# Performance work log

Measured on AMD Instinct MI355X. Metric: run time of the kernel, lower is better.

Reference implementation:

```python
import jax, jax.numpy as jnp
import numpy as np

B, S, D, H = 2, 2048, 1024, 16
DEPTH = D // H

def setup_inputs() -> dict:
    key = jax.random.key(0)
    k1, k2, k3 = jax.random.split(key, 3)
    x = jax.random.normal(k1, (B, S, D), dtype=jnp.float32)
    # causal mask (1 = attend, 0 = blocked), broadcastable over batch/heads
    mask = jnp.tril(jnp.ones((S, S), dtype=jnp.int32))[None, None]
    W_qkv = jax.random.normal(k2, (D, 3 * D), dtype=jnp.float32) * (D ** -0.5)
    b_qkv = jnp.zeros((3 * D,), dtype=jnp.float32)
    W_out = jax.random.normal(k3, (D, D), dtype=jnp.float32) * (D ** -0.5)
    b_out = jnp.zeros((D,), dtype=jnp.float32)
    return {"x": x, "mask": mask, "W_qkv": W_qkv, "b_qkv": b_qkv,
            "W_out": W_out, "b_out": b_out}

def reference(x, mask, W_qkv, b_qkv, W_out, b_out):
    b, s, _ = x.shape
    qkv = x @ W_qkv + b_qkv                        # [b, s, 3D]
    qkv = qkv.reshape(b, s, H, 3 * DEPTH)          # matches torch reshape
    qkv = jnp.transpose(qkv, (0, 2, 1, 3))         # [b, h, s, 3*depth]
    q, k, v = jnp.split(qkv, 3, axis=-1)           # each [b, h, s, depth]
    scores = jnp.einsum('bhqd,bhkd->bhqk', q, k) / jnp.sqrt(jnp.float32(DEPTH))
    scores = jnp.where(mask == 0, -jnp.inf, scores)
    attn = jax.nn.softmax(scores, axis=-1)         # dropout: eval mode (identity)
    out = jnp.einsum('bhqk,bhkd->bhqd', attn, v)   # [b, h, s, depth]
    out = jnp.transpose(out, (0, 2, 1, 3)).reshape(b, s, D)
    return out @ W_out + b_out
```

## Files before the change

kernel.cpp:

```cpp
#include <hip/hip_runtime.h>

#define BB 2
#define SS 2048
#define DDIM 1024
#define HH 16
#define DEPTH 64
#define QKVN (3*DDIM)

typedef unsigned short u16;
typedef unsigned int u32;
typedef __attribute__((ext_vector_type(8))) short bf16x8;
typedef __attribute__((ext_vector_type(4))) float f32x4;

__device__ __forceinline__ u16 f2bf(float f){
  union{float f; u32 u;} z; z.f=f;
  u32 r = z.u + 0x7fffu + ((z.u>>16)&1u);
  return (u16)(r>>16);
}
#define NEG_BIG (-1e30f)

__global__ void convT_k(const float* __restrict__ in, u16* __restrict__ out, int R, int C){
  __shared__ float tile[32][33];
  int c0 = blockIdx.x<<5, r0 = blockIdx.y<<5;
  int tx = threadIdx.x, ty = threadIdx.y;
  for (int i=ty;i<32;i+=8) tile[i][tx] = in[(size_t)(r0+i)*C + c0+tx];
  __syncthreads();
  for (int i=ty;i<32;i+=8) out[(size_t)(c0+i)*R + r0+tx] = f2bf(tile[tx][i]);
}

__global__ void convX_k(const float* __restrict__ in, u16* __restrict__ out){
  size_t i = ((size_t)blockIdx.x*256 + threadIdx.x) * 8;
  float4 a = *(const float4*)(in + i);
  float4 b = *(const float4*)(in + i + 4);
  ushort4 lo = { f2bf(a.x), f2bf(a.y), f2bf(a.z), f2bf(a.w) };
  ushort4 hi = { f2bf(b.x), f2bf(b.y), f2bf(b.z), f2bf(b.w) };
  *(ushort4*)(out + i)     = lo;
  *(ushort4*)(out + i + 4) = hi;
}

__global__ __launch_bounds__(256,2) void gemm_qkv_k(
    const u16* __restrict__ A, const u16* __restrict__ Bt,
    const float* __restrict__ bias,
    u16* __restrict__ Qb, u16* __restrict__ Kb, u16* __restrict__ Vt)
{
  const int K = DDIM;
  __shared__ __align__(16) u16 As[128*32];
  __shared__ __align__(16) u16 Bs[128*32];
  const int tid = threadIdx.x;
  const int m0 = blockIdx.x<<7, n0 = blockIdx.y<<7;
  const int w = tid>>6, lane = tid&63, q = lane>>4, ln = lane&15;
  const int wr = (w>>1)<<6, wc = (w&1)<<6;

  f32x4 acc[4][4];
  #pragma unroll
  for (int i=0;i<4;i++)
    #pragma unroll
    for (int j=0;j<4;j++) acc[i][j] = (f32x4){0.f,0.f,0.f,0.f};

  for (int k0=0;k0<K;k0+=32){
    {
      int c = tid, row = c>>2, off = (c&3)<<3;
      *(uint4*)&As[(row<<5)+off] = *(const uint4*)&A [(size_t)(m0+row)*K + k0 + off];
      *(uint4*)&Bs[(row<<5)+off] = *(const uint4*)&Bt[(size_t)(n0+row)*K + k0 + off];
      c = tid + 256; row = c>>2; off = (c&3)<<3;
      *(uint4*)&As[(row<<5)+off] = *(const uint4*)&A [(size_t)(m0+row)*K + k0 + off];
      *(uint4*)&Bs[(row<<5)+off] = *(const uint4*)&Bt[(size_t)(n0+row)*K + k0 + off];
    }
    __syncthreads();
    bf16x8 af[4], bfr[4];
    #pragma unroll
    for (int i=0;i<4;i++) af[i]  = *(const bf16x8*)&As[((wr + (i<<4) + ln)<<5) + (q<<3)];
    #pragma unroll
    for (int j=0;j<4;j++) bfr[j] = *(const bf16x8*)&Bs[((wc + (j<<4) + ln)<<5) + (q<<3)];
    #pragma unroll
    for (int i=0;i<4;i++)
      #pragma unroll
      for (int j=0;j<4;j++)
        acc[i][j] = __builtin_amdgcn_mfma_f32_16x16x32_bf16(af[i], bfr[j], acc[i][j], 0, 0, 0);
    __syncthreads();
  }

  #pragma unroll
  for (int i=0;i<4;i++){
    const int mmb = m0 + wr + (i<<4) + (q<<2);
    const int bsel = mmb >> 11;
    const int sb   = mmb & 2047;
    #pragma unroll
    for (int j=0;j<4;j++){
      const int n = n0 + wc + (j<<4) + ln;
      const int h = n / 192;
      const int rr = n - h*192;
      const int bh = (bsel<<4) + h;
      const float bv = bias[n];
      if (rr < 64){
        u16* dst = Qb + (size_t)bh*SS*DEPTH + rr;
        #pragma unroll
        for (int r=0;r<4;r++) dst[(size_t)(sb+r)*DEPTH] = f2bf((acc[i][j][r] + bv)*0.125f);
      } else if (rr < 128){
        u16* dst = Kb + (size_t)bh*SS*DEPTH + (rr-64);
        #pragma unroll
        for (int r=0;r<4;r++) dst[(size_t)(sb+r)*DEPTH] = f2bf(acc[i][j][r] + bv);
      } else {
        ushort4 pv = { f2bf(acc[i][j][0] + bv), f2bf(acc[i][j][1] + bv),
                       f2bf(acc[i][j][2] + bv), f2bf(acc[i][j][3] + bv) };
        *(ushort4*)(Vt + ((size_t)bh*DEPTH + (rr-128))*SS + sb) = pv;
      }
    }
  }
}

__global__ __launch_bounds__(256,4) void attn_k(
    u16* __restrict__ Qb, const u16* __restrict__ Kb, const u16* __restrict__ Vt)
{
  __shared__ __align__(16) u16 Ks[64*72];
  __shared__ __align__(16) u16 VsT[64*72];
  __shared__ __align__(16) u16 ps[4][16*72];

  const int tid = threadIdx.x, w = tid>>6, lane = tid&63, q = lane>>4, ln = lane&15;
  const int bh = blockIdx.x;
  const int y  = blockIdx.y, sgrp = y>>3, rr_ = y&7;
  const int qt = (sgrp==0) ? 31-rr_ : (sgrp==1) ? 16+rr_ : (sgrp==2) ? 15-rr_ : rr_;
  const int r0 = qt<<6;
  const size_t kbase = (size_t)bh*SS*DEPTH;
  const size_t vbase = (size_t)bh*DEPTH*SS;

  bf16x8 qf[2];
  #pragma unroll
  for (int ks=0;ks<2;ks++)
    qf[ks] = *(const bf16x8*)(Qb + kbase + (size_t)(r0 + (w<<4) + ln)*DEPTH + (ks<<5) + (q<<3));

  f32x4 o[4];
  #pragma unroll
  for (int nt=0;nt<4;nt++) o[nt] = (f32x4){0.f,0.f,0.f,0.f};
  float m_r[4], l_r[4];
  #pragma unroll
  for (int r=0;r<4;r++){ m_r[r] = NEG_BIG; l_r[r] = 0.f; }

  const int T = qt + 1;
  for (int t=0;t<T;t++){
    __syncthreads();
    #pragma unroll
    for (int p=0;p<2;p++){
      int e = (p*256 + tid)*8;
      int j = e>>6, d = e&63;
      *(uint4*)&Ks[j*72 + d]   = *(const uint4*)(Kb + kbase + (size_t)((t<<6)+j)*DEPTH + d);
      *(uint4*)&VsT[j*72 + d]  = *(const uint4*)(Vt + vbase + (size_t)j*SS + (t<<6) + d);
    }
    __syncthreads();

    f32x4 sc[4];
    #pragma unroll
    for (int jt=0;jt<4;jt++) sc[jt] = (f32x4){0.f,0.f,0.f,0.f};
    #pragma unroll
    for (int ks=0;ks<2;ks++){
      #pragma unroll
      for (int jt=0;jt<4;jt++){
        bf16x8 kf = *(const bf16x8*)&Ks[((jt<<4)+ln)*72 + (ks<<5) + (q<<3)];
        sc[jt] = __builtin_amdgcn_mfma_f32_16x16x32_bf16(qf[ks], kf, sc[jt], 0, 0, 0);
      }
    }

    if (t == T-1){
      const int rowb = r0 + (w<<4) + (q<<2);
      #pragma unroll
      for (int jt=0;jt<4;jt++){
        const int col = (t<<6) + (jt<<4) + ln;
        #pragma unroll
        for (int r=0;r<4;r++)
          if (col > rowb + r) sc[jt][r] = NEG_BIG;
      }
    }

    float alpha_r[4];
    #pragma unroll
    for (int r=0;r<4;r++){
      float mt = fmaxf(fmaxf(sc[0][r], sc[1][r]), fmaxf(sc[2][r], sc[3][r]));
      #pragma unroll
      for (int off=1; off<16; off<<=1) mt = fmaxf(mt, __shfl_xor(mt, off));
      const float mnew = fmaxf(m_r[r], mt);
      alpha_r[r] = __expf(m_r[r] - mnew);
      float p0 = __expf(sc[0][r]-mnew), p1 = __expf(sc[1][r]-mnew);
      float p2 = __expf(sc[2][r]-mnew), p3 = __expf(sc[3][r]-mnew);
      const int mrow = (q<<2) + r;
      ps[w][mrow*72 +      ln] = f2bf(p0);
      ps[w][mrow*72 + 16 + ln] = f2bf(p1);
      ps[w][mrow*72 + 32 + ln] = f2bf(p2);
      ps[w][mrow*72 + 48 + ln] = f2bf(p3);
      float psum = (p0+p1)+(p2+p3);
      #pragma unroll
      for (int off=1; off<16; off<<=1) psum += __shfl_xor(psum, off);
      l_r[r] = l_r[r]*alpha_r[r] + psum;
      m_r[r] = mnew;
    }
    #pragma unroll
    for (int nt=0;nt<4;nt++)
      #pragma unroll
      for (int r=0;r<4;r++) o[nt][r] *= alpha_r[r];

    __syncthreads();

    #pragma unroll
    for (int ks=0;ks<2;ks++){
      bf16x8 pa = *(const bf16x8*)&ps[w][ln*72 + (ks<<5) + (q<<3)];
      #pragma unroll
      for (int nt=0;nt<4;nt++){
        bf16x8 vf = *(const bf16x8*)&VsT[((nt<<4)+ln)*72 + (ks<<5) + (q<<3)];
        o[nt] = __builtin_amdgcn_mfma_f32_16x16x32_bf16(pa, vf, o[nt], 0, 0, 0);
      }
    }
  }

  #pragma unroll
  for (int r=0;r<4;r++){
    const float rl = 1.f / fmaxf(l_r[r], 1e-30f);
    const int s = r0 + (w<<4) + (q<<2) + r;
    #pragma unroll
    for (int nt=0;nt<4;nt++)
      Qb[kbase + (size_t)s*DEPTH + (nt<<4) + ln] = f2bf(o[nt][r] * rl);
  }
}

__global__ __launch_bounds__(256,2) void gemm_out_k(
    const u16* __restrict__ Aq, const u16* __restrict__ Bt,
    const float* __restrict__ bias, float* __restrict__ out)
{
  const int K = DDIM;
  __shared__ __align__(16) u16 As[128*32];
  __shared__ __align__(16) u16 Bs[128*32];
  const int tid = threadIdx.x;
  const int m0 = blockIdx.x<<7, n0 = blockIdx.y<<7;
  const int bsel = m0>>11, ms = m0&2047;
  const int w = tid>>6, lane = tid&63, q = lane>>4, ln = lane&15;
  const int wr = (w>>1)<<6, wc = (w&1)<<6;

  f32x4 acc[4][4];
  #pragma unroll
  for (int i=0;i<4;i++)
    #pragma unroll
    for (int j=0;j<4;j++) acc[i][j] = (f32x4){0.f,0.f,0.f,0.f};

  for (int k0=0;k0<K;k0+=32){
    const size_t abase = (size_t)((bsel<<4) + (k0>>6))*SS*DEPTH + (k0&63);
    {
      int c = tid, row = c>>2, off = (c&3)<<3;
      *(uint4*)&As[(row<<5)+off] = *(const uint4*)&Aq[abase + (size_t)(ms+row)*DEPTH + off];
      *(uint4*)&Bs[(row<<5)+off] = *(const uint4*)&Bt[(size_t)(n0+row)*K + k0 + off];
      c = tid + 256; row = c>>2; off = (c&3)<<3;
      *(uint4*)&As[(row<<5)+off] = *(const uint4*)&Aq[abase + (size_t)(ms+row)*DEPTH + off];
      *(uint4*)&Bs[(row<<5)+off] = *(const uint4*)&Bt[(size_t)(n0+row)*K + k0 + off];
    }
    __syncthreads();
    bf16x8 af[4], bfr[4];
    #pragma unroll
    for (int i=0;i<4;i++) af[i]  = *(const bf16x8*)&As[((wr + (i<<4) + ln)<<5) + (q<<3)];
    #pragma unroll
    for (int j=0;j<4;j++) bfr[j] = *(const bf16x8*)&Bs[((wc + (j<<4) + ln)<<5) + (q<<3)];
    #pragma unroll
    for (int i=0;i<4;i++)
      #pragma unroll
      for (int j=0;j<4;j++)
        acc[i][j] = __builtin_amdgcn_mfma_f32_16x16x32_bf16(af[i], bfr[j], acc[i][j], 0, 0, 0);
    __syncthreads();
  }

  #pragma unroll
  for (int i=0;i<4;i++){
    #pragma unroll
    for (int j=0;j<4;j++){
      const int n = n0 + wc + (j<<4) + ln;
      const float bv = bias[n];
      #pragma unroll
      for (int r=0;r<4;r++){
        const int mm = m0 + wr + (i<<4) + (q<<2) + r;
        out[(size_t)mm*DDIM + n] = acc[i][j][r] + bv;
      }
    }
  }
}

extern "C" void kernel_launch(void* const* d_in, const int* in_sizes, int n_in,
                              void* d_out, int out_size, void* d_ws, size_t ws_size,
                              hipStream_t stream)
{
  int ix = 0, iw = 2, ibq = 3, iwo = 4, ibo = 5;
  if (n_in == 5){ iw = 1; ibq = 2; iwo = 3; ibo = 4; }
  const float* x  = (const float*)d_in[ix];
  const float* Wq = (const float*)d_in[iw];
  const float* bq = (const float*)d_in[ibq];
  const float* Wo = (const float*)d_in[iwo];
  const float* bo = (const float*)d_in[ibo];
  float* out = (float*)d_out;

  u16* ws  = (u16*)d_ws;
  u16* Wqt = ws;
  u16* Wot = Wqt + (size_t)QKVN*DDIM;
  u16* Qb  = Wot + (size_t)DDIM*DDIM;
  u16* Kb  = Qb  + (size_t)BB*HH*SS*DEPTH;
  u16* Vt  = Kb  + (size_t)BB*HH*SS*DEPTH;
  u16* xb  = Vt  + (size_t)BB*HH*SS*DEPTH;

  convT_k<<<dim3(QKVN/32, DDIM/32), dim3(32,8), 0, stream>>>(Wq, Wqt, DDIM, QKVN);
  convT_k<<<dim3(DDIM/32, DDIM/32), dim3(32,8), 0, stream>>>(Wo, Wot, DDIM, DDIM);
  convX_k<<<dim3(BB*SS*DDIM/2048), 256, 0, stream>>>(x, xb);

  gemm_qkv_k<<<dim3(BB*SS/128, QKVN/128), 256, 0, stream>>>(xb, Wqt, bq, Qb, Kb, Vt);
  attn_k    <<<dim3(BB*HH, 32),           256, 0, stream>>>(Qb, Kb, Vt);
  gemm_out_k<<<dim3(BB*SS/128, DDIM/128), 256, 0, stream>>>(Qb, Wot, bo, out);
}
```

Before: 234.9 us.

## Use direct global-to-LDS loads in GEMMs and drop LDS staging in attention

```diff
diff --git a/kernel.cpp b/kernel.cpp
--- a/kernel.cpp
+++ b/kernel.cpp
@@ -18,6 +18,10 @@
   return (u16)(r>>16);
 }
 #define NEG_BIG (-1e30f)
+
+#define GL2LDS(gp, lp) __builtin_amdgcn_global_load_lds( \
+    (const __attribute__((address_space(1))) void*)(gp), \
+    (__attribute__((address_space(3))) void*)(lp), 16, 0, 0)
 
 __global__ void convT_k(const float* __restrict__ in, u16* __restrict__ out, int R, int C){
   __shared__ float tile[32][33];
@@ -57,15 +61,14 @@
     #pragma unroll
     for (int j=0;j<4;j++) acc[i][j] = (f32x4){0.f,0.f,0.f,0.f};
 
+  const int row0 = tid>>2,         off0 = (tid&3)<<3;
+  const int row1 = (tid+256)>>2,   off1 = (tid&3)<<3;
+
   for (int k0=0;k0<K;k0+=32){
-    {
-      int c = tid, row = c>>2, off = (c&3)<<3;
-      *(uint4*)&As[(row<<5)+off] = *(const uint4*)&A [(size_t)(m0+row)*K + k0 + off];
-      *(uint4*)&Bs[(row<<5)+off] = *(const uint4*)&Bt[(size_t)(n0+row)*K + k0 + off];
-      c = tid + 256; row = c>>2; off = (c&3)<<3;
-      *(uint4*)&As[(row<<5)+off] = *(const uint4*)&A [(size_t)(m0+row)*K + k0 + off];
-      *(uint4*)&Bs[(row<<5)+off] = *(const uint4*)&Bt[(size_t)(n0+row)*K + k0 + off];
-    }
+    GL2LDS(&A [(size_t)(m0+row0)*K + k0 + off0], &As[(row0<<5)+off0]);
+    GL2LDS(&Bt[(size_t)(n0+row0)*K + k0 + off0], &Bs[(row0<<5)+off0]);
+    GL2LDS(&A [(size_t)(m0+row1)*K + k0 + off1], &As[(row1<<5)+off1]);
+    GL2LDS(&Bt[(size_t)(n0+row1)*K + k0 + off1], &Bs[(row1<<5)+off1]);
     __syncthreads();
     bf16x8 af[4], bfr[4];
     #pragma unroll
@@ -112,8 +115,6 @@
 __global__ __launch_bounds__(256,4) void attn_k(
     u16* __restrict__ Qb, const u16* __restrict__ Kb, const u16* __restrict__ Vt)
 {
-  __shared__ __align__(16) u16 Ks[64*72];
-  __shared__ __align__(16) u16 VsT[64*72];
   __shared__ __align__(16) u16 ps[4][16*72];
 
   const int tid = threadIdx.x, w = tid>>6, lane = tid&63, q = lane>>4, ln = lane&15;
@@ -123,6 +124,8 @@
   const int r0 = qt<<6;
   const size_t kbase = (size_t)bh*SS*DEPTH;
   const size_t vbase = (size_t)bh*DEPTH*SS;
+  const u16* __restrict__ Kp = Kb + kbase;
+  const u16* __restrict__ Vp = Vt + vbase;
 
   bf16x8 qf[2];
   #pragma unroll
@@ -138,16 +141,7 @@
 
   const int T = qt + 1;
   for (int t=0;t<T;t++){
-    __syncthreads();
-    #pragma unroll
-    for (int p=0;p<2;p++){
-      int e = (p*256 + tid)*8;
-      int j = e>>6, d = e&63;
-      *(uint4*)&Ks[j*72 + d]   = *(const uint4*)(Kb + kbase + (size_t)((t<<6)+j)*DEPTH + d);
-      *(uint4*)&VsT[j*72 + d]  = *(const uint4*)(Vt + vbase + (size_t)j*SS + (t<<6) + d);
-    }
-    __syncthreads();
-
+    const u16* kp = Kp + ((size_t)(t<<6) + ln)*DEPTH + (q<<3);
     f32x4 sc[4];
     #pragma unroll
     for (int jt=0;jt<4;jt++) sc[jt] = (f32x4){0.f,0.f,0.f,0.f};
@@ -155,7 +149,7 @@
     for (int ks=0;ks<2;ks++){
       #pragma unroll
       for (int jt=0;jt<4;jt++){
-        bf16x8 kf = *(const bf16x8*)&Ks[((jt<<4)+ln)*72 + (ks<<5) + (q<<3)];
+        bf16x8 kf = *(const bf16x8*)(kp + (size_t)(jt<<4)*DEPTH + (ks<<5));
         sc[jt] = __builtin_amdgcn_mfma_f32_16x16x32_bf16(qf[ks], kf, sc[jt], 0, 0, 0);
       }
     }
@@ -197,14 +191,13 @@
       #pragma unroll
       for (int r=0;r<4;r++) o[nt][r] *= alpha_r[r];
 
-    __syncthreads();
-
+    const u16* vp = Vp + (size_t)ln*SS + (t<<6) + (q<<3);
     #pragma unroll
     for (int ks=0;ks<2;ks++){
       bf16x8 pa = *(const bf16x8*)&ps[w][ln*72 + (ks<<5) + (q<<3)];
       #pragma unroll
       for (int nt=0;nt<4;nt++){
-        bf16x8 vf = *(const bf16x8*)&VsT[((nt<<4)+ln)*72 + (ks<<5) + (q<<3)];
+        bf16x8 vf = *(const bf16x8*)(vp + (size_t)(nt<<4)*SS + (ks<<5));
         o[nt] = __builtin_amdgcn_mfma_f32_16x16x32_bf16(pa, vf, o[nt], 0, 0, 0);
       }
     }
@@ -239,16 +232,15 @@
     #pragma unroll
     for (int j=0;j<4;j++) acc[i][j] = (f32x4){0.f,0.f,0.f,0.f};
 
+  const int row0 = tid>>2,       off0 = (tid&3)<<3;
+  const int row1 = (tid+256)>>2, off1 = (tid&3)<<3;
+
   for (int k0=0;k0<K;k0+=32){
     const size_t abase = (size_t)((bsel<<4) + (k0>>6))*SS*DEPTH + (k0&63);
-    {
-      int c = tid, row = c>>2, off = (c&3)<<3;
-      *(uint4*)&As[(row<<5)+off] = *(const uint4*)&Aq[abase + (size_t)(ms+row)*DEPTH + off];
-      *(uint4*)&Bs[(row<<5)+off] = *(const uint4*)&Bt[(size_t)(n0+row)*K + k0 + off];
-      c = tid + 256; row = c>>2; off = (c&3)<<3;
-      *(uint4*)&As[(row<<5)+off] = *(const uint4*)&Aq[abase + (size_t)(ms+row)*DEPTH + off];
-      *(uint4*)&Bs[(row<<5)+off] = *(const uint4*)&Bt[(size_t)(n0+row)*K + k0 + off];
-    }
+    GL2LDS(&Aq[abase + (size_t)(ms+row0)*DEPTH + off0], &As[(row0<<5)+off0]);
+    GL2LDS(&Bt[(size_t)(n0+row0)*K + k0 + off0],        &Bs[(row0<<5)+off0]);
+    GL2LDS(&Aq[abase + (size_t)(ms+row1)*DEPTH + off1], &As[(row1<<5)+off1]);
+    GL2LDS(&Bt[(size_t)(n0+row1)*K + k0 + off1],        &Bs[(row1<<5)+off1]);
     __syncthreads();
     bf16x8 af[4], bfr[4];
     #pragma unroll
```

New measurement: 275.3 us. +17.2%, slower.
